# Performance work log

Measured on AMD Instinct MI355X. Metric: run time of the kernel, lower is better.

## Reference

```python
import jax, jax.numpy as jnp
import numpy as np

B, C_IN, C_OUT, K, IN_SIZE = 16, 32, 32, 16, 8192
OUT_SIZE = IN_SIZE - K  # 8176


def setup_inputs() -> dict:
    key = jax.random.key(0)
    kx, kw, kb = jax.random.split(key, 3)
    x = jax.random.normal(kx, (B, C_IN, IN_SIZE), dtype=jnp.float32)
    # locally-connected (non-weight-shared) conv weights generated by cppn at init
    w = jax.random.normal(kw, (C_OUT, C_IN, OUT_SIZE, K), dtype=jnp.float32)
    b = jax.random.normal(kb, (C_OUT,), dtype=jnp.float32)
    return {"x": x, "w": w, "b": b}


def reference(x, w, b):
    # sliding-window gather: idxs[o, t] = o + t, shape (O, K)
    idxs = jnp.arange(OUT_SIZE)[:, None] + jnp.arange(K)[None, :]
    windows = x[:, :, idxs]  # (B, C_in, O, K)
    # per-output-position weights: contract over C_in and K only
    out = jnp.einsum("bcok,dcok->bdo", windows, w)  # (B, C_out, O)
    return jax.nn.relu(out + b[None, :, None])
```

## Files before the change

### kernel.cpp

```cpp
#include <hip/hip_runtime.h>
#include <cstddef>

constexpr int Bn  = 16;
constexpr int CIc = 32;
constexpr int COc = 32;
constexpr int Kc  = 16;
constexpr int IN  = 8192;
constexpr int OUTL = 8176;

constexpr int O_B  = 16;
constexpr int CCH  = 8;
constexpr int NPOS = 32;
constexpr int BST  = 18;
constexpr int NCHUNK = CIc / CCH;

__global__ __launch_bounds__(256, 2)
void conv1d_cppn_kernel(const float* __restrict__ x, const float* __restrict__ w,
                        const float* __restrict__ bias, float* __restrict__ out) {
    __shared__ float xs[CCH][NPOS][BST];

    const int tid = threadIdx.x;
    const int bg  = tid & 1;
    const int ogp = (tid >> 1) & 7;
    const int dg  = tid >> 4;
    const int o0 = blockIdx.x * O_B;
    const int ob = ogp * 2;
    const int o  = o0 + ob;
    const int dbase = dg * 2;
    const int bb = bg * 8;

    const int sp4 = tid & 7;
    const int sb  = (tid >> 3) & 15;
    const int cl0 = tid >> 7;

    float acc[2][2][8];
#pragma unroll
    for (int i = 0; i < 2; ++i)
#pragma unroll
        for (int j = 0; j < 2; ++j)
#pragma unroll
            for (int q = 0; q < 8; ++q) acc[i][j][q] = 0.f;

    for (int chunk = 0; chunk < NCHUNK; ++chunk) {
        const int c0 = chunk * CCH;
        __syncthreads();
#pragma unroll
        for (int q = 0; q < 4; ++q) {
            const int cl = cl0 + 2 * q;
            const float4 v = *reinterpret_cast<const float4*>(
                &x[((size_t)sb * CIc + (c0 + cl)) * IN + o0 + sp4 * 4]);
            float (*prow)[BST] = &xs[cl][sp4 * 4];
            prow[0][sb] = v.x; prow[1][sb] = v.y; prow[2][sb] = v.z; prow[3][sb] = v.w;
        }
        __syncthreads();

#pragma unroll 2
        for (int cc = 0; cc < CCH; ++cc) {
            const int c = c0 + cc;
            float xwA[8], xwB[8];
            *reinterpret_cast<float4*>(&xwA[0]) = *reinterpret_cast<const float4*>(&xs[cc][ob][bb]);
            *reinterpret_cast<float4*>(&xwA[4]) = *reinterpret_cast<const float4*>(&xs[cc][ob][bb + 4]);
            *reinterpret_cast<float4*>(&xwB[0]) = *reinterpret_cast<const float4*>(&xs[cc][ob + 1][bb]);
            *reinterpret_cast<float4*>(&xwB[4]) = *reinterpret_cast<const float4*>(&xs[cc][ob + 1][bb + 4]);

#pragma unroll
            for (int half = 0; half < 2; ++half) {
                float wv[2][2][8];
#pragma unroll
                for (int jd = 0; jd < 2; ++jd)
#pragma unroll
                    for (int oo = 0; oo < 2; ++oo) {
                        const float4* wp = reinterpret_cast<const float4*>(
                            w + (((size_t)(dbase + jd) * CIc + c) * OUTL + (o + oo)) * Kc
                              + half * 8);
                        const float4 a  = wp[0];
                        const float4 b4 = wp[1];
                        wv[jd][oo][0] = a.x;  wv[jd][oo][1] = a.y;
                        wv[jd][oo][2] = a.z;  wv[jd][oo][3] = a.w;
                        wv[jd][oo][4] = b4.x; wv[jd][oo][5] = b4.y;
                        wv[jd][oo][6] = b4.z; wv[jd][oo][7] = b4.w;
                    }
#pragma unroll
                for (int kk = 0; kk < 8; ++kk) {
                    const int k = half * 8 + kk;
#pragma unroll
                    for (int jd = 0; jd < 2; ++jd) {
                        const float wk0 = wv[jd][0][kk];
                        const float wk1 = wv[jd][1][kk];
#pragma unroll
                        for (int j = 0; j < 8; ++j) {
                            acc[jd][0][j] += wk0 * xwA[j];
                            acc[jd][1][j] += wk1 * xwB[j];
                        }
                    }
                    if (k < 15) {
#pragma unroll
                        for (int j = 0; j < 8; ++j) xwA[j] = xwB[j];
                        const int r = ob + k + 2;
                        *reinterpret_cast<float4*>(&xwB[0]) = *reinterpret_cast<const float4*>(&xs[cc][r][bb]);
                        *reinterpret_cast<float4*>(&xwB[4]) = *reinterpret_cast<const float4*>(&xs[cc][r][bb + 4]);
                    }
                }
            }
        }
    }

#pragma unroll
    for (int jd = 0; jd < 2; ++jd) {
        const float bv = bias[dbase + jd];
#pragma unroll
        for (int j = 0; j < 8; ++j) {
            float v0 = acc[jd][0][j] + bv;
            float v1 = acc[jd][1][j] + bv;
            float2 st = make_float2(v0 > 0.f ? v0 : 0.f, v1 > 0.f ? v1 : 0.f);
            *reinterpret_cast<float2*>(
                &out[((size_t)(bb + j) * COc + (dbase + jd)) * OUTL + o]) = st;
        }
    }
}

extern "C" void kernel_launch(void* const* d_in, const int* in_sizes, int n_in,
                              void* d_out, int out_size, void* d_ws, size_t ws_size,
                              hipStream_t stream) {
    const float* x    = (const float*)d_in[0];
    const float* w    = (const float*)d_in[1];
    const float* bias = (const float*)d_in[2];
    float* out        = (float*)d_out;

    dim3 grid(OUTL / O_B);
    dim3 block(256);
    hipLaunchKernelGGL(conv1d_cppn_kernel, grid, block, 0, stream, x, w, bias, out);
}
```

Measured before the change: 151.5 us.

## Retile thread work to 4 positions x 4 batches with register-cached window rows

Changes each thread's tile from 2 output positions by 8 batch rows to 4 positions by 4 batch rows. Each half-window now loads 11 shared-memory rows into registers once, instead of sliding a two-row window. Weights are fetched as four float4 vectors per quarter of K, and outputs are written as float4 instead of float2. The shared-memory row padding goes from 18 to 20 so the float4 LDS reads stay aligned. The aim is to cut shared-memory traffic per FMA and widen stores, at the cost of more registers.

```diff
diff --git a/kernel.cpp b/kernel.cpp
--- a/kernel.cpp
+++ b/kernel.cpp
@@ -11,7 +11,7 @@
 constexpr int O_B  = 16;
 constexpr int CCH  = 8;
 constexpr int NPOS = 32;
-constexpr int BST  = 18;
+constexpr int BST  = 20;
 constexpr int NCHUNK = CIc / CCH;
 
 __global__ __launch_bounds__(256, 2)
@@ -20,26 +20,26 @@
     __shared__ float xs[CCH][NPOS][BST];
 
     const int tid = threadIdx.x;
-    const int bg  = tid & 1;
-    const int ogp = (tid >> 1) & 7;
+    const int bg  = tid & 3;
+    const int op  = (tid >> 2) & 3;
     const int dg  = tid >> 4;
     const int o0 = blockIdx.x * O_B;
-    const int ob = ogp * 2;
+    const int ob = op * 4;
     const int o  = o0 + ob;
     const int dbase = dg * 2;
-    const int bb = bg * 8;
+    const int bb = bg * 4;
 
     const int sp4 = tid & 7;
     const int sb  = (tid >> 3) & 15;
     const int cl0 = tid >> 7;
 
-    float acc[2][2][8];
+    float acc[2][4][4];
 #pragma unroll
     for (int i = 0; i < 2; ++i)
 #pragma unroll
-        for (int j = 0; j < 2; ++j)
+        for (int j = 0; j < 4; ++j)
 #pragma unroll
-            for (int q = 0; q < 8; ++q) acc[i][j][q] = 0.f;
+            for (int q = 0; q < 4; ++q) acc[i][j][q] = 0.f;
 
     for (int chunk = 0; chunk < NCHUNK; ++chunk) {
         const int c0 = chunk * CCH;
@@ -57,48 +57,40 @@
 #pragma unroll 2
         for (int cc = 0; cc < CCH; ++cc) {
             const int c = c0 + cc;
-            float xwA[8], xwB[8];
-            *reinterpret_cast<float4*>(&xwA[0]) = *reinterpret_cast<const float4*>(&xs[cc][ob][bb]);
-            *reinterpret_cast<float4*>(&xwA[4]) = *reinterpret_cast<const float4*>(&xs[cc][ob][bb + 4]);
-            *reinterpret_cast<float4*>(&xwB[0]) = *reinterpret_cast<const float4*>(&xs[cc][ob + 1][bb]);
-            *reinterpret_cast<float4*>(&xwB[4]) = *reinterpret_cast<const float4*>(&xs[cc][ob + 1][bb + 4]);
-
 #pragma unroll
             for (int half = 0; half < 2; ++half) {
-                float wv[2][2][8];
+                float rowf[11][4];
 #pragma unroll
-                for (int jd = 0; jd < 2; ++jd)
+                for (int r = 0; r < 11; ++r) {
+                    const float4 v = *reinterpret_cast<const float4*>(
+                        &xs[cc][ob + half * 8 + r][bb]);
+                    rowf[r][0] = v.x; rowf[r][1] = v.y; rowf[r][2] = v.z; rowf[r][3] = v.w;
+                }
 #pragma unroll
-                    for (int oo = 0; oo < 2; ++oo) {
-                        const float4* wp = reinterpret_cast<const float4*>(
-                            w + (((size_t)(dbase + jd) * CIc + c) * OUTL + (o + oo)) * Kc
-                              + half * 8);
-                        const float4 a  = wp[0];
-                        const float4 b4 = wp[1];
-                        wv[jd][oo][0] = a.x;  wv[jd][oo][1] = a.y;
-                        wv[jd][oo][2] = a.z;  wv[jd][oo][3] = a.w;
-                        wv[jd][oo][4] = b4.x; wv[jd][oo][5] = b4.y;
-                        wv[jd][oo][6] = b4.z; wv[jd][oo][7] = b4.w;
-                    }
+                for (int q = 0; q < 2; ++q) {
+                    float wqf[2][4][4];
 #pragma unroll
-                for (int kk = 0; kk < 8; ++kk) {
-                    const int k = half * 8 + kk;
+                    for (int jd = 0; jd < 2; ++jd)
 #pragma unroll
-                    for (int jd = 0; jd < 2; ++jd) {
-                        const float wk0 = wv[jd][0][kk];
-                        const float wk1 = wv[jd][1][kk];
+                        for (int oo = 0; oo < 4; ++oo) {
+                            const float4 v = *reinterpret_cast<const float4*>(
+                                &w[(((size_t)(dbase + jd) * CIc + c) * OUTL + (o + oo)) * Kc
+                                   + half * 8 + q * 4]);
+                            wqf[jd][oo][0] = v.x; wqf[jd][oo][1] = v.y;
+                            wqf[jd][oo][2] = v.z; wqf[jd][oo][3] = v.w;
+                        }
 #pragma unroll
-                        for (int j = 0; j < 8; ++j) {
-                            acc[jd][0][j] += wk0 * xwA[j];
-                            acc[jd][1][j] += wk1 * xwB[j];
-                        }
-                    }
-                    if (k < 15) {
+                    for (int kk = 0; kk < 4; ++kk) {
+                        const int lr = q * 4 + kk;
 #pragma unroll
-                        for (int j = 0; j < 8; ++j) xwA[j] = xwB[j];
-                        const int r = ob + k + 2;
-                        *reinterpret_cast<float4*>(&xwB[0]) = *reinterpret_cast<const float4*>(&xs[cc][r][bb]);
-                        *reinterpret_cast<float4*>(&xwB[4]) = *reinterpret_cast<const float4*>(&xs[cc][r][bb + 4]);
+                        for (int jd = 0; jd < 2; ++jd)
+#pragma unroll
+                            for (int oo = 0; oo < 4; ++oo) {
+                                const float wk = wqf[jd][oo][kk];
+#pragma unroll
+                                for (int j = 0; j < 4; ++j)
+                                    acc[jd][oo][j] += wk * rowf[lr + oo][j];
+                            }
                     }
                 }
             }
@@ -109,11 +101,17 @@
     for (int jd = 0; jd < 2; ++jd) {
         const float bv = bias[dbase + jd];
 #pragma unroll
-        for (int j = 0; j < 8; ++j) {
+        for (int j = 0; j < 4; ++j) {
+            float4 st;
             float v0 = acc[jd][0][j] + bv;
             float v1 = acc[jd][1][j] + bv;
-            float2 st = make_float2(v0 > 0.f ? v0 : 0.f, v1 > 0.f ? v1 : 0.f);
-            *reinterpret_cast<float2*>(
+            float v2 = acc[jd][2][j] + bv;
+            float v3 = acc[jd][3][j] + bv;
+            st.x = v0 > 0.f ? v0 : 0.f;
+            st.y = v1 > 0.f ? v1 : 0.f;
+            st.z = v2 > 0.f ? v2 : 0.f;
+            st.w = v3 > 0.f ? v3 : 0.f;
+            *reinterpret_cast<float4*>(
                 &out[((size_t)(bb + j) * COc + (dbase + jd)) * OUTL + o]) = st;
         }
     }
```

After: 218.7 us. +44.4%, slower.

## Reorder shared x tile into even/odd halves and batch-load window rows

Applied to the files above, without the earlier changes.

The shared x tile is stored with a padded row stride and its rows permuted so even positions sit in the first half and odd positions in the second. This is meant to cut LDS bank conflicts when neighbouring output groups read rows. All 16 K-weights per (d, o) are now loaded at the start of each channel, and a 9-row window of x is preloaded into registers per half instead of shifting row by row. The cc loop is no longer unrolled, which lowers code size but raises register pressure under launch bounds (256,2). It also drops the cross-iteration overlap that the old unroll-by-2 gave.

```diff
diff --git a/kernel.cpp b/kernel.cpp
--- a/kernel.cpp
+++ b/kernel.cpp
@@ -11,8 +11,9 @@
 constexpr int O_B  = 16;
 constexpr int CCH  = 8;
 constexpr int NPOS = 32;
-constexpr int BST  = 18;
+constexpr int BST  = 20;
 constexpr int NCHUNK = CIc / CCH;
+
 
 __global__ __launch_bounds__(256, 2)
 void conv1d_cppn_kernel(const float* __restrict__ x, const float* __restrict__ w,
@@ -49,57 +50,57 @@
             const int cl = cl0 + 2 * q;
             const float4 v = *reinterpret_cast<const float4*>(
                 &x[((size_t)sb * CIc + (c0 + cl)) * IN + o0 + sp4 * 4]);
-            float (*prow)[BST] = &xs[cl][sp4 * 4];
-            prow[0][sb] = v.x; prow[1][sb] = v.y; prow[2][sb] = v.z; prow[3][sb] = v.w;
+            xs[cl][sp4 * 2 + 0 ][sb] = v.x;
+            xs[cl][sp4 * 2 + 16][sb] = v.y;
+            xs[cl][sp4 * 2 + 1 ][sb] = v.z;
+            xs[cl][sp4 * 2 + 17][sb] = v.w;
         }
         __syncthreads();
 
-#pragma unroll 2
+#pragma unroll 1
         for (int cc = 0; cc < CCH; ++cc) {
             const int c = c0 + cc;
-            float xwA[8], xwB[8];
-            *reinterpret_cast<float4*>(&xwA[0]) = *reinterpret_cast<const float4*>(&xs[cc][ob][bb]);
-            *reinterpret_cast<float4*>(&xwA[4]) = *reinterpret_cast<const float4*>(&xs[cc][ob][bb + 4]);
-            *reinterpret_cast<float4*>(&xwB[0]) = *reinterpret_cast<const float4*>(&xs[cc][ob + 1][bb]);
-            *reinterpret_cast<float4*>(&xwB[4]) = *reinterpret_cast<const float4*>(&xs[cc][ob + 1][bb + 4]);
+            float wreg[2][2][16];
+#pragma unroll
+            for (int jd = 0; jd < 2; ++jd)
+#pragma unroll
+                for (int oo = 0; oo < 2; ++oo) {
+                    const float4* wp = reinterpret_cast<const float4*>(
+                        w + (((size_t)(dbase + jd) * CIc + c) * OUTL + (o + oo)) * Kc);
+#pragma unroll
+                    for (int q = 0; q < 4; ++q) {
+                        const float4 v = wp[q];
+                        wreg[jd][oo][q * 4 + 0] = v.x;
+                        wreg[jd][oo][q * 4 + 1] = v.y;
+                        wreg[jd][oo][q * 4 + 2] = v.z;
+                        wreg[jd][oo][q * 4 + 3] = v.w;
+                    }
+                }
 
 #pragma unroll
-            for (int half = 0; half < 2; ++half) {
-                float wv[2][2][8];
+            for (int h = 0; h < 2; ++h) {
+                float xr[9][8];
+                const int eb = ogp + 4 * h;
+                const int obs = 16 + ogp + 4 * h;
 #pragma unroll
-                for (int jd = 0; jd < 2; ++jd)
-#pragma unroll
-                    for (int oo = 0; oo < 2; ++oo) {
-                        const float4* wp = reinterpret_cast<const float4*>(
-                            w + (((size_t)(dbase + jd) * CIc + c) * OUTL + (o + oo)) * Kc
-                              + half * 8);
-                        const float4 a  = wp[0];
-                        const float4 b4 = wp[1];
-                        wv[jd][oo][0] = a.x;  wv[jd][oo][1] = a.y;
-                        wv[jd][oo][2] = a.z;  wv[jd][oo][3] = a.w;
-                        wv[jd][oo][4] = b4.x; wv[jd][oo][5] = b4.y;
-                        wv[jd][oo][6] = b4.z; wv[jd][oo][7] = b4.w;
-                    }
+                for (int lr = 0; lr < 9; ++lr) {
+                    const int pr = (lr & 1) ? (obs + (lr >> 1)) : (eb + (lr >> 1));
+                    const float* src = &xs[cc][pr][bb];
+                    *reinterpret_cast<float4*>(&xr[lr][0]) = *reinterpret_cast<const float4*>(src);
+                    *reinterpret_cast<float4*>(&xr[lr][4]) = *reinterpret_cast<const float4*>(src + 4);
+                }
 #pragma unroll
                 for (int kk = 0; kk < 8; ++kk) {
-                    const int k = half * 8 + kk;
 #pragma unroll
-                    for (int jd = 0; jd < 2; ++jd) {
-                        const float wk0 = wv[jd][0][kk];
-                        const float wk1 = wv[jd][1][kk];
+                    for (int jd = 0; jd < 2; ++jd)
 #pragma unroll
-                        for (int j = 0; j < 8; ++j) {
-                            acc[jd][0][j] += wk0 * xwA[j];
-                            acc[jd][1][j] += wk1 * xwB[j];
+                        for (int oo = 0; oo < 2; ++oo) {
+                            const float wk = wreg[jd][oo][h * 8 + kk];
+                            const float* xv = &xr[kk + oo][0];
+#pragma unroll
+                            for (int j = 0; j < 8; ++j)
+                                acc[jd][oo][j] += wk * xv[j];
                         }
-                    }
-                    if (k < 15) {
-#pragma unroll
-                        for (int j = 0; j < 8; ++j) xwA[j] = xwB[j];
-                        const int r = ob + k + 2;
-                        *reinterpret_cast<float4*>(&xwB[0]) = *reinterpret_cast<const float4*>(&xs[cc][r][bb]);
-                        *reinterpret_cast<float4*>(&xwB[4]) = *reinterpret_cast<const float4*>(&xs[cc][r][bb + 4]);
-                    }
                 }
             }
         }
```

Result: faster. 137.3 us (-9.4%).
